# Kernel tuning notes

Measured on AMD Instinct MI355X. Metric: run time of the kernel, lower is better.

## Reference

```python
import jax, jax.numpy as jnp
import numpy as np
from functools import partial

DELTA_B = 30.0
DELTA_H = 30.0
NB = 12  # 360/30
NH = 12
E, H, A, MLP, T = 16, 32, 32, 128, 20


def setup_inputs() -> dict:
    key = jax.random.key(0)
    ks = jax.random.split(key, 32)
    B, N = 512, 32
    inp = {}
    inp['x'] = jax.random.normal(ks[0], (B, N, T, 2), jnp.float32)
    inp['dmat'] = jax.random.uniform(ks[1], (B, N, T, N), jnp.float32) * 10.0
    inp['bmat'] = jax.random.uniform(ks[2], (B, N, T, N), jnp.float32) * 360.0
    inp['hmat'] = jax.random.uniform(ks[3], (B, N, T, N), jnp.float32) * 360.0
    inp['mask'] = jnp.ones((B, N, T), jnp.float32)
    g = lambda k, sh, s=0.1: jax.random.normal(k, sh, jnp.float32) * s
    inp['emb_w'] = g(ks[4], (2, E)); inp['emb_b'] = jnp.zeros((E,), jnp.float32)
    inp['w_ih'] = g(ks[5], (E, 4 * H)); inp['w_hh'] = g(ks[6], (H, 4 * H))
    inp['b_ih'] = jnp.zeros((4 * H,), jnp.float32); inp['b_hh'] = jnp.zeros((4 * H,), jnp.float32)
    inp['enc2att_w'] = g(ks[7], (H, A)); inp['enc2att_b'] = jnp.zeros((A,), jnp.float32)
    inp['domain_tab'] = jnp.full((NB, NH), 5.0, jnp.float32)  # domain_parameter init
    inp['spemb_w'] = g(ks[8], (2 * A, A)); inp['spemb_b'] = jnp.zeros((A,), jnp.float32)
    inp['att2enc_w'] = g(ks[9], (A, H)); inp['att2enc_b'] = jnp.zeros((H,), jnp.float32)
    inp['cls_w1'] = g(ks[10], (T * H, MLP)); inp['cls_b1'] = jnp.zeros((MLP,), jnp.float32)
    inp['cls_w2'] = g(ks[11], (MLP, MLP)); inp['cls_b2'] = jnp.zeros((MLP,), jnp.float32)
    inp['cls_w3'] = g(ks[12], (MLP, 1)); inp['cls_b3'] = jnp.zeros((1,), jnp.float32)
    return inp


def _forward(x, dmat, bmat, hmat, mask, emb_w, emb_b, w_ih, w_hh, b_ih, b_hh,
             enc2att_w, enc2att_b, domain_tab, spemb_w, spemb_b,
             att2enc_w, att2enc_b, cls_w1, cls_b1, cls_w2, cls_b2, cls_w3, cls_b3):
    B, N = x.shape[0], x.shape[1]
    xe = x @ emb_w + emb_b                      # [B,N,T,E]
    # time-major sequences for scan
    seq = (jnp.moveaxis(xe, 2, 0), jnp.moveaxis(dmat, 2, 0), jnp.moveaxis(bmat, 2, 0),
           jnp.moveaxis(hmat, 2, 0), jnp.moveaxis(mask, 2, 0))
    h0 = jnp.zeros((B, N, H), xe.dtype)
    c0 = jnp.zeros((B, N, H), xe.dtype)

    def step(carry, inp):
        h, c = carry
        x_t, d_t, b_t, hd_t, m_t = inp
        gates = x_t @ w_ih + h @ w_hh + (b_ih + b_hh)   # [B,N,4H]
        i, f, g, o = jnp.split(gates, 4, axis=-1)
        c_new = jax.nn.sigmoid(f) * c + jax.nn.sigmoid(i) * jnp.tanh(g)
        h_lstm = jax.nn.sigmoid(o) * jnp.tanh(c_new)
        ha = h_lstm @ enc2att_w + enc2att_b              # enc2att -> [B,N,A]
        # spatial attention: domain value from bearing/heading bins vs distance
        ib = jnp.clip(jnp.floor(b_t / DELTA_B), 0, NB - 1).astype(jnp.int32)
        ih = jnp.clip(jnp.floor(hd_t / DELTA_H), 0, NH - 1).astype(jnp.int32)
        w = jax.nn.relu(domain_tab[ib, ih] - d_t)        # [B,N,N]
        w = w * m_t[:, :, None] * m_t[:, None, :]
        w = w / (w.sum(-1, keepdims=True) + 1e-8)
        att = jnp.einsum('bij,bjd->bid', w, ha)          # neighbor-weighted hidden
        emb = jnp.tanh(jnp.concatenate([ha, att], -1) @ spemb_w + spemb_b)
        h_new = emb @ att2enc_w + att2enc_b              # back to hidden_size
        return (h_new, c_new), h_new

    (_, _), hs = jax.lax.scan(step, (h0, c0), seq)       # hs: [T,B,N,H]
    enc = jnp.moveaxis(hs, 0, 2).reshape(B, N, T * H)
    z = jax.nn.leaky_relu(enc @ cls_w1 + cls_b1, 0.2)
    z = jax.nn.leaky_relu(z @ cls_w2 + cls_b2, 0.2)
    return jax.nn.sigmoid(z @ cls_w3 + cls_b3)           # [B,N,1]


def reference(x, dmat, bmat, hmat, mask, emb_w, emb_b, w_ih, w_hh, b_ih, b_hh,
              enc2att_w, enc2att_b, domain_tab, spemb_w, spemb_b,
              att2enc_w, att2enc_b, cls_w1, cls_b1, cls_w2, cls_b2, cls_w3, cls_b3):
    return _forward(x, dmat, bmat, hmat, mask, emb_w, emb_b, w_ih, w_hh, b_ih, b_hh,
                    enc2att_w, enc2att_b, domain_tab, spemb_w, spemb_b,
                    att2enc_w, att2enc_b, cls_w1, cls_b1, cls_w2, cls_b2, cls_w3, cls_b3)
```

## Files before the change

### kernel.cpp

```cpp
#include <hip/hip_runtime.h>
#include <hip/hip_bf16.h>

#define TD_B 512

typedef __bf16 bf16x8 __attribute__((ext_vector_type(8)));
typedef __bf16 bf16x4 __attribute__((ext_vector_type(4)));
typedef float  f32x4  __attribute__((ext_vector_type(4)));

#define MFMA(a, b, c) __builtin_amdgcn_mfma_f32_16x16x32_bf16((a), (b), (c), 0, 0, 0)

__device__ __forceinline__ float sigf(float x)  { return 1.0f / (1.0f + __expf(-x)); }
__device__ __forceinline__ float tanhf_(float x){ return 2.0f / (1.0f + __expf(-2.0f * x)) - 1.0f; }

__device__ __forceinline__ void sync_lds() {
    __builtin_amdgcn_sched_barrier(0);
    asm volatile("s_waitcnt lgkmcnt(0)" ::: "memory");
    __builtin_amdgcn_s_barrier();
    __builtin_amdgcn_sched_barrier(0);
}

extern "C" __global__ void __launch_bounds__(256, 2)
traj_disc_kernel(const float* __restrict__ x, const float* __restrict__ dmat,
                 const float* __restrict__ bmat, const float* __restrict__ hmat,
                 const float* __restrict__ mask,
                 const float* __restrict__ emb_w, const float* __restrict__ emb_b,
                 const float* __restrict__ w_ih, const float* __restrict__ w_hh,
                 const float* __restrict__ b_ih, const float* __restrict__ b_hh,
                 const float* __restrict__ e2a_w, const float* __restrict__ e2a_b,
                 const float* __restrict__ dom,
                 const float* __restrict__ sp_w, const float* __restrict__ sp_b,
                 const float* __restrict__ a2e_w, const float* __restrict__ a2e_b,
                 const float* __restrict__ w1, const float* __restrict__ b1,
                 const float* __restrict__ w2, const float* __restrict__ b2,
                 const float* __restrict__ w3, const float* __restrict__ b3,
                 float* __restrict__ out)
{
    const int b    = blockIdx.x;
    const int tid  = threadIdx.x;
    const int lane = tid & 63;
    const int w    = tid >> 6;
    const int l15  = lane & 15;
    const int lg   = lane >> 4;

    __shared__ __bf16 sAin[32][72];
    __shared__ __bf16 sHl [32][40];
    __shared__ __bf16 sWN [32][40];
    __shared__ __bf16 sVT [32][40];
    __shared__ __bf16 sEmb[32][40];
    __shared__ float  sMaskT[20][36];
    __shared__ float  sDom[144];
    __shared__ float  sRS[32];
    __shared__ float  sE1[32][33];
    __shared__ float  sE2[32][33];
    __shared__ float  sBu[32], sBv[32];
    __shared__ __bf16 z1bf[32][136];
    __shared__ __bf16 z2bf[32][136];
    __shared__ int    sFlag;

    if (tid == 0) sFlag = 1;
    for (int idx = tid; idx < 32 * 72; idx += 256)
        (&sAin[0][0])[idx] = (idx % 72 == 48) ? (__bf16)1.0f : (__bf16)0.0f;
    for (int idx = tid; idx < 640; idx += 256) {
        int tt = idx >> 5, n = idx & 31;
        sMaskT[tt][n] = mask[(b * 32 + n) * 20 + tt];
    }
    if (tid < 144) sDom[tid] = dom[tid];
    for (int idx = tid; idx < 1024; idx += 256) {
        int k = idx >> 5, c = idx & 31;
        float a1 = 0.f, a2 = 0.f;
        #pragma unroll 4
        for (int j = 0; j < 32; ++j) {
            float e = e2a_w[k * 32 + j];
            a1 += e * sp_w[j * 32 + c];
            a2 += e * sp_w[(32 + j) * 32 + c];
        }
        sE1[k][c] = a1; sE2[k][c] = a2;
    }
    if (tid < 32) {
        float s1 = 0.f, s2 = 0.f;
        #pragma unroll 4
        for (int k = 0; k < 32; ++k) {
            float e = e2a_b[k];
            s1 += e * sp_w[k * 32 + tid];
            s2 += e * sp_w[(32 + k) * 32 + tid];
        }
        sBu[tid] = s1 + sp_b[tid];
        sBv[tid] = s2;
    }
    __syncthreads();
    {
        const float d0 = sDom[0];
        bool ok = true;
        for (int i = tid; i < 144; i += 256) ok &= (sDom[i] == d0);
        for (int i = tid; i < 640; i += 256) ok &= ((&sMaskT[0][0])[(i >> 5) * 36 + (i & 31)] == 1.0f);
        if (!ok) sFlag = 0;
    }

    const int i0 = tid >> 3, p0 = tid & 7;
    const float dom0 = dom[0];
    const float ewa0 = emb_w[2 * p0],      ewa1 = emb_w[2 * p0 + 1];
    const float ewb0 = emb_w[16 + 2 * p0], ewb1 = emb_w[16 + 2 * p0 + 1];
    const float eb0  = emb_b[2 * p0],      eb1  = emb_b[2 * p0 + 1];

    bf16x8 Ag[2][2];
    #pragma unroll
    for (int mtl = 0; mtl < 2; ++mtl) {
        int c  = (2 * w + mtl) * 16 + l15;
        int cg = (c & 3) * 32 + (c >> 2);
        #pragma unroll
        for (int kt = 0; kt < 2; ++kt)
            #pragma unroll
            for (int j = 0; j < 8; ++j) {
                int k = kt * 32 + lg * 8 + j;
                float v;
                if (k < 16)       v = w_ih[k * 128 + cg];
                else if (k < 48)  v = w_hh[(k - 16) * 128 + cg];
                else if (k == 48) v = b_ih[cg] + b_hh[cg];
                else              v = 0.0f;
                Ag[mtl][kt][j] = (__bf16)v;
            }
    }
    const int mtw = w >> 1, ntw = w & 1;
    const int cw  = ntw * 16 + l15;
    bf16x8 BE1, BE2, Ba2e;
    #pragma unroll
    for (int j = 0; j < 8; ++j) {
        BE1[j]  = (__bf16)sE1[lg * 8 + j][cw];
        BE2[j]  = (__bf16)sE2[lg * 8 + j][cw];
        Ba2e[j] = (__bf16)a2e_w[(lg * 8 + j) * 32 + cw];
    }
    const float buw = sBu[cw], bvw = sBv[cw], bAw = a2e_b[cw];

    float cst[2][2] = {{0.f, 0.f}, {0.f, 0.f}};
    f32x4 accZ[2][2] = {};
    bf16x8 Bw1cur[2];

    const float* dp = dmat + ((long)(b * 32 + i0) * 20) * 32 + 4 * p0;
    const float* bp = bmat + ((long)(b * 32 + i0) * 20) * 32 + 4 * p0;
    const float* hp = hmat + ((long)(b * 32 + i0) * 20) * 32 + 4 * p0;
    const float* xp = x + ((long)(b * 32 + i0) * 20) * 2;
    const float* w1p = w1 + lg * 8 * 128 + 32 * w + l15;

    float4 pdv = *(const float4*)dp;
    float4 pbv = *(const float4*)bp;
    float4 phv = *(const float4*)hp;
    float px0 = xp[0], px1 = xp[1];
    __syncthreads();
    const bool fast = (sFlag != 0);

    #pragma unroll 1
    for (int t = 0; t < 20; ++t) {
        {
            float4 dv = pdv, bv = pbv, hv = phv;
            float xx0 = px0, xx1 = px1;
            if (t < 19) {
                pdv = *(const float4*)(dp + 32); dp += 32;
                if (!fast) {
                    pbv = *(const float4*)(bp + 32); bp += 32;
                    phv = *(const float4*)(hp + 32); hp += 32;
                }
                px0 = xp[2]; px1 = xp[3]; xp += 2;
            }
            float wq[4];
            float inv, s;
            if (fast) {
                #pragma unroll
                for (int q = 0; q < 4; ++q) {
                    float v = dom0 - (&dv.x)[q];
                    wq[q] = v > 0.f ? v : 0.f;
                }
                s = wq[0] + wq[1] + wq[2] + wq[3];
                s += __shfl_xor(s, 1); s += __shfl_xor(s, 2); s += __shfl_xor(s, 4);
                inv = 1.0f / (s + 1e-8f);
            } else {
                float4 mj = *(const float4*)&sMaskT[t][4 * p0];
                float  mi = sMaskT[t][i0];
                #pragma unroll
                for (int q = 0; q < 4; ++q) {
                    float bq = (&bv.x)[q], hq = (&hv.x)[q];
                    int ib = (int)floorf(bq * (1.0f / 30.0f)); ib = ib < 0 ? 0 : (ib > 11 ? 11 : ib);
                    int ih = (int)floorf(hq * (1.0f / 30.0f)); ih = ih < 0 ? 0 : (ih > 11 ? 11 : ih);
                    float v = sDom[ib * 12 + ih] - (&dv.x)[q];
                    v = v > 0.f ? v : 0.f;
                    wq[q] = v * (&mj.x)[q];
                }
                s = wq[0] + wq[1] + wq[2] + wq[3];
                s += __shfl_xor(s, 1); s += __shfl_xor(s, 2); s += __shfl_xor(s, 4);
                inv = mi / (mi * s + 1e-8f);
            }
            bf16x4 wn4;
            #pragma unroll
            for (int q = 0; q < 4; ++q) wn4[q] = (__bf16)(wq[q] * inv);
            *(bf16x4*)&sWN[i0][4 * p0] = wn4;
            if (p0 == 0) sRS[i0] = s * inv;
            sAin[i0][2 * p0]     = (__bf16)(xx0 * ewa0 + xx1 * ewb0 + eb0);
            sAin[i0][2 * p0 + 1] = (__bf16)(xx0 * ewa1 + xx1 * ewb1 + eb1);
        }
        sync_lds();

        {
            bf16x8 bxh[2][2];
            #pragma unroll
            for (int nt = 0; nt < 2; ++nt)
                #pragma unroll
                for (int kt = 0; kt < 2; ++kt)
                    bxh[nt][kt] = *(const bf16x8*)&sAin[nt * 16 + l15][kt * 32 + lg * 8];
            if (t >= 1) {
                bf16x8 az[2];
                #pragma unroll
                for (int mt = 0; mt < 2; ++mt)
                    az[mt] = *(const bf16x8*)&sAin[mt * 16 + l15][16 + lg * 8];
                #pragma unroll
                for (int mt = 0; mt < 2; ++mt)
                    #pragma unroll
                    for (int ntp = 0; ntp < 2; ++ntp)
                        accZ[mt][ntp] = MFMA(az[mt], Bw1cur[ntp], accZ[mt][ntp]);
            }
            #pragma unroll
            for (int mtl = 0; mtl < 2; ++mtl)
                #pragma unroll
                for (int nt = 0; nt < 2; ++nt) {
                    f32x4 cc = {0.f, 0.f, 0.f, 0.f};
                    cc = MFMA(Ag[mtl][0], bxh[nt][0], cc);
                    cc = MFMA(Ag[mtl][1], bxh[nt][1], cc);
                    float cn = sigf(cc[1]) * cst[mtl][nt] + sigf(cc[0]) * tanhf_(cc[2]);
                    cst[mtl][nt] = cn;
                    sHl[nt * 16 + l15][4 * (2 * w + mtl) + lg] = (__bf16)(sigf(cc[3]) * tanhf_(cn));
                }
            #pragma unroll
            for (int ntp = 0; ntp < 2; ++ntp)
                #pragma unroll
                for (int j = 0; j < 8; ++j)
                    Bw1cur[ntp][j] = (__bf16)w1p[j * 128 + ntp * 16];
            w1p += 4096;
        }
        sync_lds();

        f32x4 ureg;
        {
            bf16x8 a = *(const bf16x8*)&sHl[mtw * 16 + l15][lg * 8];
            f32x4 cu = {0.f, 0.f, 0.f, 0.f};
            ureg = MFMA(a, BE1, cu);
            f32x4 cv = {0.f, 0.f, 0.f, 0.f};
            cv = MFMA(a, BE2, cv);
            bf16x4 tv;
            #pragma unroll
            for (int q = 0; q < 4; ++q) tv[q] = (__bf16)cv[q];
            *(bf16x4*)&sVT[cw][mtw * 16 + 4 * lg] = tv;
        }
        sync_lds();

        {
            bf16x8 aW = *(const bf16x8*)&sWN[mtw * 16 + l15][lg * 8];
            bf16x8 bT = *(const bf16x8*)&sVT[cw][lg * 8];
            f32x4 cc = {0.f, 0.f, 0.f, 0.f};
            cc = MFMA(aW, bT, cc);
            #pragma unroll
            for (int q = 0; q < 4; ++q) {
                float rsv = sRS[mtw * 16 + 4 * lg + q];
                sEmb[mtw * 16 + 4 * lg + q][cw] =
                    (__bf16)tanhf_(ureg[q] + cc[q] + rsv * bvw + buw);
            }
        }
        sync_lds();

        {
            bf16x8 a = *(const bf16x8*)&sEmb[mtw * 16 + l15][lg * 8];
            f32x4 cc = {0.f, 0.f, 0.f, 0.f};
            cc = MFMA(a, Ba2e, cc);
            #pragma unroll
            for (int q = 0; q < 4; ++q)
                sAin[mtw * 16 + 4 * lg + q][16 + cw] = (__bf16)(cc[q] + bAw);
        }
    }

    __syncthreads();
    {
        bf16x8 az[2];
        #pragma unroll
        for (int mt = 0; mt < 2; ++mt)
            az[mt] = *(const bf16x8*)&sAin[mt * 16 + l15][16 + lg * 8];
        #pragma unroll
        for (int mt = 0; mt < 2; ++mt)
            #pragma unroll
            for (int ntp = 0; ntp < 2; ++ntp)
                accZ[mt][ntp] = MFMA(az[mt], Bw1cur[ntp], accZ[mt][ntp]);
    }
    #pragma unroll
    for (int mt = 0; mt < 2; ++mt)
        #pragma unroll
        for (int ntp = 0; ntp < 2; ++ntp) {
            int c = (2 * w + ntp) * 16 + l15;
            float bias = b1[c];
            #pragma unroll
            for (int q = 0; q < 4; ++q) {
                float v = accZ[mt][ntp][q] + bias;
                v = v > 0.f ? v : 0.2f * v;
                z1bf[mt * 16 + 4 * lg + q][c] = (__bf16)v;
            }
        }
    __syncthreads();

    {
        f32x4 c2[2][2] = {};
        #pragma unroll
        for (int kt = 0; kt < 4; ++kt) {
            bf16x8 a[2];
            #pragma unroll
            for (int mt = 0; mt < 2; ++mt)
                a[mt] = *(const bf16x8*)&z1bf[mt * 16 + l15][kt * 32 + lg * 8];
            bf16x8 bb[2];
            #pragma unroll
            for (int ntp = 0; ntp < 2; ++ntp) {
                int c = (2 * w + ntp) * 16 + l15;
                #pragma unroll
                for (int j = 0; j < 8; ++j)
                    bb[ntp][j] = (__bf16)w2[(kt * 32 + lg * 8 + j) * 128 + c];
            }
            #pragma unroll
            for (int mt = 0; mt < 2; ++mt)
                #pragma unroll
                for (int ntp = 0; ntp < 2; ++ntp)
                    c2[mt][ntp] = MFMA(a[mt], bb[ntp], c2[mt][ntp]);
        }
        #pragma unroll
        for (int mt = 0; mt < 2; ++mt)
            #pragma unroll
            for (int ntp = 0; ntp < 2; ++ntp) {
                int c = (2 * w + ntp) * 16 + l15;
                float bias = b2[c];
                #pragma unroll
                for (int q = 0; q < 4; ++q) {
                    float v = c2[mt][ntp][q] + bias;
                    v = v > 0.f ? v : 0.2f * v;
                    z2bf[mt * 16 + 4 * lg + q][c] = (__bf16)v;
                }
            }
    }
    __syncthreads();

    {
        int n = tid >> 3, kg = tid & 7;
        bf16x8 v0 = *(const bf16x8*)&z2bf[n][kg * 16];
        bf16x8 v1 = *(const bf16x8*)&z2bf[n][kg * 16 + 8];
        float s = 0.f;
        #pragma unroll
        for (int j = 0; j < 8; ++j)
            s += (float)v0[j] * w3[kg * 16 + j] + (float)v1[j] * w3[kg * 16 + 8 + j];
        s += __shfl_xor(s, 1); s += __shfl_xor(s, 2); s += __shfl_xor(s, 4);
        if (kg == 0) out[b * 32 + n] = sigf(s + b3[0]);
    }
}

extern "C" void kernel_launch(void* const* d_in, const int* in_sizes, int n_in,
                              void* d_out, int out_size, void* d_ws, size_t ws_size,
                              hipStream_t stream) {
    (void)in_sizes; (void)n_in; (void)d_ws; (void)ws_size; (void)out_size;
    const float* x     = (const float*)d_in[0];
    const float* dmat  = (const float*)d_in[1];
    const float* bmat  = (const float*)d_in[2];
    const float* hmat  = (const float*)d_in[3];
    const float* mask  = (const float*)d_in[4];
    const float* emb_w = (const float*)d_in[5];
    const float* emb_b = (const float*)d_in[6];
    const float* w_ih  = (const float*)d_in[7];
    const float* w_hh  = (const float*)d_in[8];
    const float* b_ih  = (const float*)d_in[9];
    const float* b_hh  = (const float*)d_in[10];
    const float* e2a_w = (const float*)d_in[11];
    const float* e2a_b = (const float*)d_in[12];
    const float* dom   = (const float*)d_in[13];
    const float* sp_w  = (const float*)d_in[14];
    const float* sp_b  = (const float*)d_in[15];
    const float* a2e_w = (const float*)d_in[16];
    const float* a2e_b = (const float*)d_in[17];
    const float* w1    = (const float*)d_in[18];
    const float* b1    = (const float*)d_in[19];
    const float* w2    = (const float*)d_in[20];
    const float* b2    = (const float*)d_in[21];
    const float* w3    = (const float*)d_in[22];
    const float* b3    = (const float*)d_in[23];
    float* out = (float*)d_out;

    traj_disc_kernel<<<dim3(TD_B), dim3(256), 0, stream>>>(
        x, dmat, bmat, hmat, mask, emb_w, emb_b, w_ih, w_hh, b_ih, b_hh,
        e2a_w, e2a_b, dom, sp_w, sp_b, a2e_w, a2e_b,
        w1, b1, w2, b2, w3, b3, out);
}
```

Baseline: 73.68 us.

## Merge attention stages per wave to drop barriers and prefetch next-step weights

Each wave now redundantly computes the full V projection and the full 32-column attention embedding for its row half. The V-projection, attention and att2enc stages therefore run without block-wide barriers between them, cutting per-step LDS barriers from four to two. The neighbor-weight preparation for step t+1 is moved to the end of step t, with sWN and sRS double-buffered, so it overlaps the tail of the current step. The cost is more MFMA work and LDS writes per wave, plus several waves writing the same shared values.

```diff
diff --git a/kernel.cpp b/kernel.cpp
--- a/kernel.cpp
+++ b/kernel.cpp
@@ -44,12 +44,12 @@
 
     __shared__ __bf16 sAin[32][72];
     __shared__ __bf16 sHl [32][40];
-    __shared__ __bf16 sWN [32][40];
+    __shared__ __bf16 sWN [2][32][40];
     __shared__ __bf16 sVT [32][40];
     __shared__ __bf16 sEmb[32][40];
     __shared__ float  sMaskT[20][36];
     __shared__ float  sDom[144];
-    __shared__ float  sRS[32];
+    __shared__ float  sRS[2][32];
     __shared__ float  sE1[32][33];
     __shared__ float  sE2[32][33];
     __shared__ float  sBu[32], sBv[32];
@@ -122,80 +122,90 @@
     }
     const int mtw = w >> 1, ntw = w & 1;
     const int cw  = ntw * 16 + l15;
-    bf16x8 BE1, BE2, Ba2e;
+    bf16x8 BE1[2], BE2[2], Ba2e;
+    float bu2[2], bv2[2];
     #pragma unroll
-    for (int j = 0; j < 8; ++j) {
-        BE1[j]  = (__bf16)sE1[lg * 8 + j][cw];
-        BE2[j]  = (__bf16)sE2[lg * 8 + j][cw];
+    for (int nt = 0; nt < 2; ++nt) {
+        int c2 = nt * 16 + l15;
+        #pragma unroll
+        for (int j = 0; j < 8; ++j) {
+            BE1[nt][j] = (__bf16)sE1[lg * 8 + j][c2];
+            BE2[nt][j] = (__bf16)sE2[lg * 8 + j][c2];
+        }
+        bu2[nt] = sBu[c2];
+        bv2[nt] = sBv[c2];
+    }
+    #pragma unroll
+    for (int j = 0; j < 8; ++j)
         Ba2e[j] = (__bf16)a2e_w[(lg * 8 + j) * 32 + cw];
-    }
-    const float buw = sBu[cw], bvw = sBv[cw], bAw = a2e_b[cw];
+    const float bAw = a2e_b[cw];
 
     float cst[2][2] = {{0.f, 0.f}, {0.f, 0.f}};
     f32x4 accZ[2][2] = {};
     bf16x8 Bw1cur[2];
 
-    const float* dp = dmat + ((long)(b * 32 + i0) * 20) * 32 + 4 * p0;
-    const float* bp = bmat + ((long)(b * 32 + i0) * 20) * 32 + 4 * p0;
-    const float* hp = hmat + ((long)(b * 32 + i0) * 20) * 32 + 4 * p0;
-    const float* xp = x + ((long)(b * 32 + i0) * 20) * 2;
+    const float* dp  = dmat + ((long)(b * 32 + i0) * 20) * 32 + 4 * p0;
+    const float* bp0 = bmat + ((long)(b * 32 + i0) * 20) * 32 + 4 * p0;
+    const float* hp0 = hmat + ((long)(b * 32 + i0) * 20) * 32 + 4 * p0;
+    const float* xp  = x + ((long)(b * 32 + i0) * 20) * 2;
     const float* w1p = w1 + lg * 8 * 128 + 32 * w + l15;
 
     float4 pdv = *(const float4*)dp;
-    float4 pbv = *(const float4*)bp;
-    float4 phv = *(const float4*)hp;
     float px0 = xp[0], px1 = xp[1];
     __syncthreads();
     const bool fast = (sFlag != 0);
 
+    auto phaseA = [&](int tt) {
+        float4 dv = pdv;
+        float xx0 = px0, xx1 = px1;
+        if (tt < 19) {
+            pdv = *(const float4*)(dp + 32); dp += 32;
+            px0 = xp[2]; px1 = xp[3]; xp += 2;
+        }
+        float wq[4];
+        float inv, s;
+        if (fast) {
+            #pragma unroll
+            for (int q = 0; q < 4; ++q) {
+                float v = dom0 - (&dv.x)[q];
+                wq[q] = v > 0.f ? v : 0.f;
+            }
+            s = wq[0] + wq[1] + wq[2] + wq[3];
+            s += __shfl_xor(s, 1); s += __shfl_xor(s, 2); s += __shfl_xor(s, 4);
+            inv = 1.0f / (s + 1e-8f);
+        } else {
+            const float* bb2 = bp0 + 32 * tt;
+            const float* hh2 = hp0 + 32 * tt;
+            float4 bv = *(const float4*)bb2;
+            float4 hv = *(const float4*)hh2;
+            float4 mj = *(const float4*)&sMaskT[tt][4 * p0];
+            float  mi = sMaskT[tt][i0];
+            #pragma unroll
+            for (int q = 0; q < 4; ++q) {
+                float bq = (&bv.x)[q], hq = (&hv.x)[q];
+                int ib = (int)floorf(bq * (1.0f / 30.0f)); ib = ib < 0 ? 0 : (ib > 11 ? 11 : ib);
+                int ih = (int)floorf(hq * (1.0f / 30.0f)); ih = ih < 0 ? 0 : (ih > 11 ? 11 : ih);
+                float v = sDom[ib * 12 + ih] - (&dv.x)[q];
+                v = v > 0.f ? v : 0.f;
+                wq[q] = v * (&mj.x)[q];
+            }
+            s = wq[0] + wq[1] + wq[2] + wq[3];
+            s += __shfl_xor(s, 1); s += __shfl_xor(s, 2); s += __shfl_xor(s, 4);
+            inv = mi / (mi * s + 1e-8f);
+        }
+        bf16x4 wn4;
+        #pragma unroll
+        for (int q = 0; q < 4; ++q) wn4[q] = (__bf16)(wq[q] * inv);
+        *(bf16x4*)&sWN[tt & 1][i0][4 * p0] = wn4;
+        if (p0 == 0) sRS[tt & 1][i0] = s * inv;
+        sAin[i0][2 * p0]     = (__bf16)(xx0 * ewa0 + xx1 * ewb0 + eb0);
+        sAin[i0][2 * p0 + 1] = (__bf16)(xx0 * ewa1 + xx1 * ewb1 + eb1);
+    };
+
+    phaseA(0);
+
     #pragma unroll 1
     for (int t = 0; t < 20; ++t) {
-        {
-            float4 dv = pdv, bv = pbv, hv = phv;
-            float xx0 = px0, xx1 = px1;
-            if (t < 19) {
-                pdv = *(const float4*)(dp + 32); dp += 32;
-                if (!fast) {
-                    pbv = *(const float4*)(bp + 32); bp += 32;
-                    phv = *(const float4*)(hp + 32); hp += 32;
-                }
-                px0 = xp[2]; px1 = xp[3]; xp += 2;
-            }
-            float wq[4];
-            float inv, s;
-            if (fast) {
-                #pragma unroll
-                for (int q = 0; q < 4; ++q) {
-                    float v = dom0 - (&dv.x)[q];
-                    wq[q] = v > 0.f ? v : 0.f;
-                }
-                s = wq[0] + wq[1] + wq[2] + wq[3];
-                s += __shfl_xor(s, 1); s += __shfl_xor(s, 2); s += __shfl_xor(s, 4);
-                inv = 1.0f / (s + 1e-8f);
-            } else {
-                float4 mj = *(const float4*)&sMaskT[t][4 * p0];
-                float  mi = sMaskT[t][i0];
-                #pragma unroll
-                for (int q = 0; q < 4; ++q) {
-                    float bq = (&bv.x)[q], hq = (&hv.x)[q];
-                    int ib = (int)floorf(bq * (1.0f / 30.0f)); ib = ib < 0 ? 0 : (ib > 11 ? 11 : ib);
-                    int ih = (int)floorf(hq * (1.0f / 30.0f)); ih = ih < 0 ? 0 : (ih > 11 ? 11 : ih);
-                    float v = sDom[ib * 12 + ih] - (&dv.x)[q];
-                    v = v > 0.f ? v : 0.f;
-                    wq[q] = v * (&mj.x)[q];
-                }
-                s = wq[0] + wq[1] + wq[2] + wq[3];
-                s += __shfl_xor(s, 1); s += __shfl_xor(s, 2); s += __shfl_xor(s, 4);
-                inv = mi / (mi * s + 1e-8f);
-            }
-            bf16x4 wn4;
-            #pragma unroll
-            for (int q = 0; q < 4; ++q) wn4[q] = (__bf16)(wq[q] * inv);
-            *(bf16x4*)&sWN[i0][4 * p0] = wn4;
-            if (p0 == 0) sRS[i0] = s * inv;
-            sAin[i0][2 * p0]     = (__bf16)(xx0 * ewa0 + xx1 * ewb0 + eb0);
-            sAin[i0][2 * p0 + 1] = (__bf16)(xx0 * ewa1 + xx1 * ewb1 + eb1);
-        }
         sync_lds();
 
         {
@@ -236,42 +246,47 @@
         }
         sync_lds();
 
-        f32x4 ureg;
         {
-            bf16x8 a = *(const bf16x8*)&sHl[mtw * 16 + l15][lg * 8];
-            f32x4 cu = {0.f, 0.f, 0.f, 0.f};
-            ureg = MFMA(a, BE1, cu);
-            f32x4 cv = {0.f, 0.f, 0.f, 0.f};
-            cv = MFMA(a, BE2, cv);
-            bf16x4 tv;
-            #pragma unroll
-            for (int q = 0; q < 4; ++q) tv[q] = (__bf16)cv[q];
-            *(bf16x4*)&sVT[cw][mtw * 16 + 4 * lg] = tv;
-        }
-        sync_lds();
-
-        {
-            bf16x8 aW = *(const bf16x8*)&sWN[mtw * 16 + l15][lg * 8];
-            bf16x8 bT = *(const bf16x8*)&sVT[cw][lg * 8];
-            f32x4 cc = {0.f, 0.f, 0.f, 0.f};
-            cc = MFMA(aW, bT, cc);
-            #pragma unroll
-            for (int q = 0; q < 4; ++q) {
-                float rsv = sRS[mtw * 16 + 4 * lg + q];
-                sEmb[mtw * 16 + 4 * lg + q][cw] =
-                    (__bf16)tanhf_(ureg[q] + cc[q] + rsv * bvw + buw);
-            }
-        }
-        sync_lds();
-
-        {
-            bf16x8 a = *(const bf16x8*)&sEmb[mtw * 16 + l15][lg * 8];
-            f32x4 cc = {0.f, 0.f, 0.f, 0.f};
-            cc = MFMA(a, Ba2e, cc);
+            bf16x8 aHl0 = *(const bf16x8*)&sHl[l15][lg * 8];
+            bf16x8 aHl1 = *(const bf16x8*)&sHl[16 + l15][lg * 8];
+            f32x4 zero = {0.f, 0.f, 0.f, 0.f};
+            f32x4 cv[2][2];
+            cv[0][0] = MFMA(aHl0, BE2[0], zero);
+            cv[0][1] = MFMA(aHl0, BE2[1], zero);
+            cv[1][0] = MFMA(aHl1, BE2[0], zero);
+            cv[1][1] = MFMA(aHl1, BE2[1], zero);
+            bf16x8 aMt = mtw ? aHl1 : aHl0;
+            f32x4 uc[2];
+            uc[0] = MFMA(aMt, BE1[0], zero);
+            uc[1] = MFMA(aMt, BE1[1], zero);
+            #pragma unroll
+            for (int mt = 0; mt < 2; ++mt)
+                #pragma unroll
+                for (int nt = 0; nt < 2; ++nt) {
+                    bf16x4 tv;
+                    #pragma unroll
+                    for (int q = 0; q < 4; ++q) tv[q] = (__bf16)cv[mt][nt][q];
+                    *(bf16x4*)&sVT[nt * 16 + l15][mt * 16 + 4 * lg] = tv;
+                }
+            bf16x8 wNf = *(const bf16x8*)&sWN[t & 1][mtw * 16 + l15][lg * 8];
+            bf16x8 bT0 = *(const bf16x8*)&sVT[l15][lg * 8];
+            bf16x8 bT1 = *(const bf16x8*)&sVT[16 + l15][lg * 8];
+            uc[0] = MFMA(wNf, bT0, uc[0]);
+            uc[1] = MFMA(wNf, bT1, uc[1]);
+            float4 rs4 = *(const float4*)&sRS[t & 1][mtw * 16 + 4 * lg];
+            #pragma unroll
+            for (int nt = 0; nt < 2; ++nt)
+                #pragma unroll
+                for (int q = 0; q < 4; ++q)
+                    sEmb[mtw * 16 + 4 * lg + q][nt * 16 + l15] =
+                        (__bf16)tanhf_(uc[nt][q] + (&rs4.x)[q] * bv2[nt] + bu2[nt]);
+            bf16x8 aE = *(const bf16x8*)&sEmb[mtw * 16 + l15][lg * 8];
+            f32x4 cf = MFMA(aE, Ba2e, zero);
             #pragma unroll
             for (int q = 0; q < 4; ++q)
-                sAin[mtw * 16 + 4 * lg + q][16 + cw] = (__bf16)(cc[q] + bAw);
-        }
+                sAin[mtw * 16 + 4 * lg + q][16 + cw] = (__bf16)(cf[q] + bAw);
+        }
+        if (t < 19) phaseA(t + 1);
     }
 
     __syncthreads();
```

Result: slower. 81.33 us (+10.4%).
